# Kernel tuning notes

Measured on AMD Instinct MI355X. Metric: run time of the kernel, lower is better.

Reference implementation:

```python
import jax, jax.numpy as jnp
from jax import lax
import numpy as np

D_MODEL = 2048
NUM_EXPERTS = 16
NUM_TOKENS = 8192  # must be divisible by NUM_EXPERTS (balanced assignment)


def setup_inputs() -> dict:
    key = jax.random.key(0)
    k1, k2 = jax.random.split(key)
    features = jax.random.normal(k1, (NUM_TOKENS, D_MODEL), dtype=jnp.float32)
    # gate weight (orthogonal init in torch; gaussian is fine for a numerical baseline)
    W = jax.random.normal(k2, (NUM_EXPERTS, D_MODEL), dtype=jnp.float32) * 0.1
    b = jnp.zeros((NUM_EXPERTS,), dtype=jnp.float32)
    return {"features": features, "W": W, "b": b, "is_training": 1}


def _balanced_assignment(scores):
    """Greedy balanced assignment: each expert receives exactly T//E tokens.
    Deterministic stand-in for the cpp auction-based balanced_assignment: scan
    over tokens, each token takes its best-scoring expert with remaining capacity.
    Returns sort_by_expert: token indices sorted (stably) by assigned expert."""
    T, E = scores.shape
    cap_per_expert = T // E

    def step(cap, s):  # cap: [E] remaining capacity, s: [E] token's scores
        masked = jnp.where(cap > 0, s, -jnp.inf)
        e = jnp.argmax(masked)
        return cap.at[e].add(-1), e

    _, tok2exp = lax.scan(step, jnp.full((E,), cap_per_expert, dtype=jnp.int32), scores)
    sort_by_expert = jnp.argsort(tok2exp, stable=True)  # [T] token ids grouped by expert
    return sort_by_expert


def reference(features, W, b, is_training):
    # gating computed under no_grad in the original
    affinities = lax.stop_gradient(features @ W.T + b)  # [T, E]
    T, E = affinities.shape
    cap = T // E

    sort_by_expert = _balanced_assignment(affinities)

    routing_probs = jax.nn.softmax(affinities, axis=1)  # [T, E]

    # gather_scores: permute probs into expert order, pick each token's score for
    # its assigned expert, then un-permute back to original token order.
    sorted_probs = routing_probs[sort_by_expert]                 # [T, E]
    expert_idx = (jnp.arange(T) // cap)[:, None]                 # [T, 1], balanced splits
    gathered = jnp.take_along_axis(sorted_probs, expert_idx, axis=1)  # [T, 1]
    i_sort = jnp.argsort(sort_by_expert)                         # inverse permutation
    gathered_scores = gathered[i_sort]                           # [T, 1]

    return sort_by_expert, gathered_scores
```

## Files before the change

### kernel.cpp

```cpp
#include <hip/hip_runtime.h>
#include <hip/hip_bf16.h>
#include <math.h>

#define T_TOK 8192
#define D_MODEL 2048
#define N_EXP 16
#define CAP 512
#define NSEG (T_TOK / 64)


__device__ __forceinline__ unsigned int f2ord(float f) {
    unsigned int b = __float_as_uint(f);
    return (b & 0x80000000u) ? ~b : (b | 0x80000000u);
}

__global__ __launch_bounds__(512, 4) void gemm_aff_kernel(
    const float* __restrict__ feat, const float* __restrict__ W,
    float* __restrict__ aff)
{
    __shared__ float flds[8][D_MODEL];

    const int tid  = threadIdx.x;
    const int wave = tid >> 6, lane = tid & 63;
    const int tbase = blockIdx.x * 8;

    {
        const float4* src = (const float4*)(feat + (size_t)tbase * D_MODEL);
        float4* dst = (float4*)&flds[0][0];
        #pragma unroll
        for (int i = 0; i < 8; ++i)
            dst[tid + i * 512] = src[tid + i * 512];
    }

    const float* w0 = W + (size_t)(wave * 2) * D_MODEL + lane * 4;
    const float* w1 = w0 + D_MODEL;

    float acc[16];
    #pragma unroll
    for (int i = 0; i < 16; ++i) acc[i] = 0.f;

    float4 wv0 = *(const float4*)(w0);
    float4 wv1 = *(const float4*)(w1);
    __syncthreads();

    #pragma unroll
    for (int j = 0; j < 8; ++j) {
        float4 wn0, wn1;
        if (j < 7) {
            wn0 = *(const float4*)(w0 + (j + 1) * 256);
            wn1 = *(const float4*)(w1 + (j + 1) * 256);
        } else {
            wn0 = wv0; wn1 = wv1;
        }
        const float* fl = &flds[0][0] + j * 256 + lane * 4;
        #pragma unroll
        for (int r = 0; r < 8; ++r) {
            float4 f = *(const float4*)(fl + r * D_MODEL);
            acc[r * 2 + 0] += f.x * wv0.x;
            acc[r * 2 + 0] += f.y * wv0.y;
            acc[r * 2 + 0] += f.z * wv0.z;
            acc[r * 2 + 0] += f.w * wv0.w;
            acc[r * 2 + 1] += f.x * wv1.x;
            acc[r * 2 + 1] += f.y * wv1.y;
            acc[r * 2 + 1] += f.z * wv1.z;
            acc[r * 2 + 1] += f.w * wv1.w;
        }
        wv0 = wn0; wv1 = wn1;
    }

    #pragma unroll
    for (int step = 0; step < 4; ++step) {
        const int m    = 1 << step;
        const int half = 8 >> step;
        const bool hi  = (lane & m) != 0;
        #pragma unroll
        for (int jj = 0; jj < half; ++jj) {
            float send = hi ? acc[jj] : acc[jj + half];
            float recv = __shfl_xor(send, m, 64);
            acc[jj] = (hi ? acc[jj + half] : acc[jj]) + recv;
        }
    }
    acc[0] += __shfl_xor(acc[0], 16, 64);
    acc[0] += __shfl_xor(acc[0], 32, 64);

    if (lane < 16) {
        const int slot = ((lane & 1) << 3) | (((lane >> 1) & 1) << 2)
                       | (((lane >> 2) & 1) << 1) | ((lane >> 3) & 1);
        const int r = slot >> 1, el = slot & 1;
        aff[(size_t)(tbase + r) * N_EXP + wave * 2 + el] = acc[0];
    }
}

__global__ __launch_bounds__(256) void finalize_kernel(
    const float* __restrict__ aff_in, const float* __restrict__ bias,
    unsigned long long* __restrict__ pref, float* __restrict__ probs)
{
    const int t = blockIdx.x * 256 + threadIdx.x;

    float aff[N_EXP];
    const float4* p = (const float4*)(aff_in + (size_t)t * N_EXP);
    #pragma unroll
    for (int q = 0; q < 4; ++q) {
        float4 v = p[q];
        aff[q*4+0] = v.x; aff[q*4+1] = v.y; aff[q*4+2] = v.z; aff[q*4+3] = v.w;
    }
    #pragma unroll
    for (int e = 0; e < N_EXP; ++e) aff[e] += bias[e];

    float m = aff[0];
    #pragma unroll
    for (int e = 1; e < N_EXP; ++e) m = fmaxf(m, aff[e]);
    float s = 0.f;
    #pragma unroll
    for (int e = 0; e < N_EXP; ++e) s += __expf(aff[e] - m);

    float4* pr = (float4*)(probs + (size_t)t * N_EXP);
    #pragma unroll
    for (int q = 0; q < 4; ++q) {
        float4 v;
        v.x = __expf(aff[q*4+0] - m) / s;
        v.y = __expf(aff[q*4+1] - m) / s;
        v.z = __expf(aff[q*4+2] - m) / s;
        v.w = __expf(aff[q*4+3] - m) / s;
        pr[q] = v;
    }

    unsigned long long key[N_EXP];
    #pragma unroll
    for (int j = 0; j < N_EXP; ++j)
        key[j] = ((unsigned long long)f2ord(aff[j]) << 4) | (unsigned long long)(15 - j);
    unsigned long long pk = 0ull;
    unsigned int used = 0;
    for (int r = 0; r < N_EXP; ++r) {
        unsigned long long bk = 0ull; int be = 0;
        for (int j = 0; j < N_EXP; ++j)
            if (!((used >> j) & 1u) && key[j] > bk) { bk = key[j]; be = j; }
        used |= (1u << be);
        pk = (pk << 4) | (unsigned long long)be;
    }
    pref[t] = pk;
}

__global__ __launch_bounds__(512, 1) void events_kernel(
    const unsigned long long* __restrict__ pref, int* __restrict__ evt)
{
    __shared__ unsigned long long segmask[N_EXP][NSEG];
    __shared__ int fparr[N_EXP];

    const int tid  = threadIdx.x;
    const int wave = tid >> 6, lane = tid & 63;
    const unsigned long long lt_mask = (1ull << lane) - 1ull;

    unsigned long long myPref[16];
    #pragma unroll
    for (int k = 0; k < 16; ++k) myPref[k] = pref[tid + 512 * k];

    #pragma unroll
    for (int k = 0; k < 16; ++k) {
        const int s = k * 8 + wave;
        const int c = (int)(myPref[k] >> 60);
        #pragma unroll
        for (int e = 0; e < N_EXP; ++e) {
            unsigned long long mm = __ballot(c == e);
            if (lane == e) segmask[e][s] = mm;
        }
    }
    __syncthreads();

    const int eA = wave, eB = wave + 8;
    int capA = CAP, capB = CAP;
    unsigned long long m0A = 0, m1A = 0, m0B = 0, m1B = 0;
    int excl0A = 0, excl1A = 0, excl0B = 0, excl1B = 0;
    int segF = 0;
    unsigned long long mlep = 0;
    unsigned int avail = 0xFFFFu;
    int myp = 0, myf = 0;

    for (int round = 0; round < N_EXP; ++round) {
        {
            int exf = (segF < 64) ? __shfl(excl0A, segF, 64) : __shfl(excl1A, segF - 64, 64);
            unsigned long long mf = (segF < 64) ? __shfl(m0A, segF, 64) : __shfl(m1A, segF - 64, 64);
            capA -= exf + (int)__popcll(mf & mlep);
            exf = (segF < 64) ? __shfl(excl0B, segF, 64) : __shfl(excl1B, segF - 64, 64);
            mf  = (segF < 64) ? __shfl(m0B, segF, 64) : __shfl(m1B, segF - 64, 64);
            capB -= exf + (int)__popcll(mf & mlep);
        }

        unsigned long long a0 = segmask[eA][lane];
        unsigned long long a1 = segmask[eA][64 + lane];
        unsigned long long b0 = segmask[eB][lane];
        unsigned long long b1 = segmask[eB][64 + lane];
        if (lane < segF)            { a0 = 0; b0 = 0; }
        else if (lane == segF)      { a0 &= ~mlep; b0 &= ~mlep; }
        if (64 + lane < segF)       { a1 = 0; b1 = 0; }
        else if (64 + lane == segF) { a1 &= ~mlep; b1 &= ~mlep; }
        m0A = a0; m1A = a1; m0B = b0; m1B = b1;

        const int c0A = (int)__popcll(a0), c1A = (int)__popcll(a1);
        const int c0B = (int)__popcll(b0), c1B = (int)__popcll(b1);
        int v0A = c0A, v1A = c1A, v0B = c0B, v1B = c1B;
        #pragma unroll
        for (int d = 1; d < 64; d <<= 1) {
            int t0 = __shfl_up(v0A, d, 64);
            int t1 = __shfl_up(v1A, d, 64);
            int t2 = __shfl_up(v0B, d, 64);
            int t3 = __shfl_up(v1B, d, 64);
            if (lane >= d) { v0A += t0; v1A += t1; v0B += t2; v1B += t3; }
        }
        const int tot0A = __shfl(v0A, 63, 64);
        const int tot0B = __shfl(v0B, 63, 64);
        excl0A = v0A - c0A;
        excl1A = tot0A + v1A - c1A;
        excl0B = v0B - c0B;
        excl1B = tot0B + v1B - c1B;

        int fpA = 0x7FFFFFFF;
        if ((avail >> eA) & 1u) {
            const int need = capA;
            int segc = -1, kk = 0;
            if (excl0A < need && excl0A + c0A >= need)      { segc = lane;      kk = need - excl0A; }
            else if (excl1A < need && excl1A + c1A >= need) { segc = 64 + lane; kk = need - excl1A; }
            unsigned long long bb = __ballot(segc >= 0);
            if (bb) {
                int l2    = __builtin_ctzll(bb);
                int sstar = __shfl(segc, l2, 64);
                int k2    = __shfl(kk,   l2, 64);
                unsigned long long msel = (sstar < 64) ? __shfl(a0, sstar, 64)
                                                       : __shfl(a1, sstar - 64, 64);
                int rr = (int)__popcll(msel & lt_mask);
                bool hit = ((msel >> lane) & 1ull) && (rr == k2 - 1);
                unsigned long long hb = __ballot(hit);
                fpA = sstar * 64 + __builtin_ctzll(hb);
            }
        }
        int fpB = 0x7FFFFFFF;
        if ((avail >> eB) & 1u) {
            const int need = capB;
            int segc = -1, kk = 0;
            if (excl0B < need && excl0B + c0B >= need)      { segc = lane;      kk = need - excl0B; }
            else if (excl1B < need && excl1B + c1B >= need) { segc = 64 + lane; kk = need - excl1B; }
            unsigned long long bb = __ballot(segc >= 0);
            if (bb) {
                int l2    = __builtin_ctzll(bb);
                int sstar = __shfl(segc, l2, 64);
                int k2    = __shfl(kk,   l2, 64);
                unsigned long long msel = (sstar < 64) ? __shfl(b0, sstar, 64)
                                                       : __shfl(b1, sstar - 64, 64);
                int rr = (int)__popcll(msel & lt_mask);
                bool hit = ((msel >> lane) & 1ull) && (rr == k2 - 1);
                unsigned long long hb = __ballot(hit);
                fpB = sstar * 64 + __builtin_ctzll(hb);
            }
        }
        if (lane == 0) { fparr[eA] = fpA; fparr[eB] = fpB; }
        __syncthreads();

        int pmin = 0x7FFFFFFF, fe = 0;
        #pragma unroll
        for (int e = 0; e < N_EXP; ++e) {
            int f = fparr[e];
            if (f < pmin) { pmin = f; fe = e; }
        }
        if (tid == round) { myp = pmin; myf = fe; }

        const int nsegF = pmin >> 6;
        const unsigned long long nmlep = ((pmin & 63) == 63) ? ~0ull
                                         : ((1ull << ((pmin & 63) + 1)) - 1ull);
        const unsigned int navail = avail & ~(1u << fe);

        if (round < N_EXP - 1) {
            #pragma unroll
            for (int k = 0; k < 16; ++k) {
                const int s = k * 8 + wave;
                if (s >= nsegF) {
                    unsigned long long m = segmask[fe][s];
                    if (s == nsegF) m &= ~nmlep;
                    if ((m >> lane) & 1ull) {
                        unsigned long long pp = myPref[k];
                        int e2 = (int)(pp >> 60);
                        while (!((navail >> e2) & 1u)) { pp <<= 4; e2 = (int)(pp >> 60); }
                        atomicOr(&segmask[e2][s], 1ull << lane);
                    }
                }
            }
        }
        segF = nsegF; mlep = nmlep; avail = navail;
        __syncthreads();
    }

    if (tid < N_EXP) { evt[tid] = myp; evt[N_EXP + tid] = myf; }
}

__global__ __launch_bounds__(256) void choice_kernel(
    const unsigned long long* __restrict__ pref, const int* __restrict__ evt,
    unsigned char* __restrict__ t2e, int* __restrict__ bcnt)
{
    __shared__ int evp[N_EXP], evf[N_EXP];
    __shared__ int sc[4][N_EXP];
    const int tid = threadIdx.x, b = blockIdx.x;
    const int wave = tid >> 6, lane = tid & 63;
    if (tid < N_EXP) evp[tid] = evt[tid];
    else if (tid < 2 * N_EXP) evf[tid - N_EXP] = evt[tid];
    __syncthreads();

    const int t = b * 256 + tid;
    unsigned int mask = 0xFFFFu;
    #pragma unroll
    for (int j = 0; j < N_EXP; ++j)
        if (evp[j] < t) mask &= ~(1u << evf[j]);

    unsigned long long pp = pref[t];
    int e = (int)(pp >> 60);
    while (!((mask >> e) & 1u)) { pp <<= 4; e = (int)(pp >> 60); }
    t2e[t] = (unsigned char)e;

    #pragma unroll
    for (int e2 = 0; e2 < N_EXP; ++e2) {
        unsigned long long mm = __ballot(e == e2);
        if (lane == e2) sc[wave][e2] = (int)__popcll(mm);
    }
    __syncthreads();
    if (tid < N_EXP)
        bcnt[b * N_EXP + tid] = sc[0][tid] + sc[1][tid] + sc[2][tid] + sc[3][tid];
}

__global__ __launch_bounds__(256) void writeout_kernel(
    const unsigned char* __restrict__ t2e, const int* __restrict__ bcnt,
    const float* __restrict__ probs,
    float* __restrict__ out0, float* __restrict__ out1)
{
    __shared__ int base[N_EXP];
    __shared__ int sc[4][N_EXP];
    const int tid = threadIdx.x, b = blockIdx.x;
    const int wave = tid >> 6, lane = tid & 63;
    const unsigned long long lt_mask = (1ull << lane) - 1ull;

    const int t = b * 256 + tid;
    const int c = (int)t2e[t];

    unsigned long long own = 0ull;
    #pragma unroll
    for (int e2 = 0; e2 < N_EXP; ++e2) {
        unsigned long long mm = __ballot(c == e2);
        if (c == e2) own = mm;
        if (lane == e2) sc[wave][e2] = (int)__popcll(mm);
    }
    if (tid < N_EXP) {
        int s = 0;
        for (int b2 = 0; b2 < b; ++b2) s += bcnt[b2 * N_EXP + tid];
        base[tid] = s;
    }
    __syncthreads();

    int rank = (int)__popcll(own & lt_mask);
    for (int w2 = 0; w2 < wave; ++w2) rank += sc[w2][c];
    const int pos = base[c] + rank;
    out0[c * CAP + pos] = (float)t;
    out1[t] = probs[(size_t)t * N_EXP + c];
}

extern "C" void kernel_launch(void* const* d_in, const int* in_sizes, int n_in,
                              void* d_out, int out_size, void* d_ws, size_t ws_size,
                              hipStream_t stream) {
    const float* feat = (const float*)d_in[0];
    const float* W    = (const float*)d_in[1];
    const float* bias = (const float*)d_in[2];

    float* out = (float*)d_out;
    char*  ws  = (char*)d_ws;

    float* aff               = (float*)ws;
    unsigned long long* pref = (unsigned long long*)(ws + 524288);
    float* probs             = (float*)(ws + 589824);
    int* evt                 = (int*)(ws + 1114112);
    unsigned char* t2e       = (unsigned char*)(ws + 1114240);
    int* bcnt                = (int*)(ws + 1122432);

    hipLaunchKernelGGL(gemm_aff_kernel, dim3(T_TOK / 8), dim3(512), 0, stream,
                       feat, W, aff);
    hipLaunchKernelGGL(finalize_kernel, dim3(T_TOK / 256), dim3(256), 0, stream,
                       aff, bias, pref, probs);
    hipLaunchKernelGGL(events_kernel, dim3(1), dim3(512), 0, stream,
                       pref, evt);
    hipLaunchKernelGGL(choice_kernel, dim3(T_TOK / 256), dim3(256), 0, stream,
                       pref, evt, t2e, bcnt);
    hipLaunchKernelGGL(writeout_kernel, dim3(T_TOK / 256), dim3(256), 0, stream,
                       t2e, bcnt, probs, out, out + T_TOK);
}
```

Baseline: 185.6 us.

## Fuse softmax/preference into GEMM and merge choice with writeout via grid sync

```diff
diff --git a/kernel.cpp b/kernel.cpp
--- a/kernel.cpp
+++ b/kernel.cpp
@@ -14,11 +14,13 @@
     return (b & 0x80000000u) ? ~b : (b | 0x80000000u);
 }
 
-__global__ __launch_bounds__(512, 4) void gemm_aff_kernel(
+__global__ __launch_bounds__(512, 4) void gemm_finalize_kernel(
     const float* __restrict__ feat, const float* __restrict__ W,
-    float* __restrict__ aff)
+    const float* __restrict__ bias,
+    unsigned long long* __restrict__ pref, float* __restrict__ probs)
 {
     __shared__ float flds[8][D_MODEL];
+    __shared__ float afft[8][N_EXP];
 
     const int tid  = threadIdx.x;
     const int wave = tid >> 6, lane = tid & 63;
@@ -87,62 +89,48 @@
         const int slot = ((lane & 1) << 3) | (((lane >> 1) & 1) << 2)
                        | (((lane >> 2) & 1) << 1) | ((lane >> 3) & 1);
         const int r = slot >> 1, el = slot & 1;
-        aff[(size_t)(tbase + r) * N_EXP + wave * 2 + el] = acc[0];
-    }
-}
-
-__global__ __launch_bounds__(256) void finalize_kernel(
-    const float* __restrict__ aff_in, const float* __restrict__ bias,
-    unsigned long long* __restrict__ pref, float* __restrict__ probs)
-{
-    const int t = blockIdx.x * 256 + threadIdx.x;
-
-    float aff[N_EXP];
-    const float4* p = (const float4*)(aff_in + (size_t)t * N_EXP);
-    #pragma unroll
-    for (int q = 0; q < 4; ++q) {
-        float4 v = p[q];
-        aff[q*4+0] = v.x; aff[q*4+1] = v.y; aff[q*4+2] = v.z; aff[q*4+3] = v.w;
-    }
-    #pragma unroll
-    for (int e = 0; e < N_EXP; ++e) aff[e] += bias[e];
-
-    float m = aff[0];
-    #pragma unroll
-    for (int e = 1; e < N_EXP; ++e) m = fmaxf(m, aff[e]);
+        afft[r][wave * 2 + el] = acc[0];
+    }
+    __syncthreads();
+
+    const int tk = tbase + wave;
+    const int j  = lane & 15;
+    float v = afft[wave][j] + bias[j];
+
+    float mx = v;
+    #pragma unroll
+    for (int d = 1; d < 16; d <<= 1)
+        mx = fmaxf(mx, __shfl_xor(mx, d, 16));
+
+    float ex = __expf(v - mx);
+
     float s = 0.f;
     #pragma unroll
-    for (int e = 0; e < N_EXP; ++e) s += __expf(aff[e] - m);
-
-    float4* pr = (float4*)(probs + (size_t)t * N_EXP);
-    #pragma unroll
-    for (int q = 0; q < 4; ++q) {
-        float4 v;
-        v.x = __expf(aff[q*4+0] - m) / s;
-        v.y = __expf(aff[q*4+1] - m) / s;
-        v.z = __expf(aff[q*4+2] - m) / s;
-        v.w = __expf(aff[q*4+3] - m) / s;
-        pr[q] = v;
-    }
-
-    unsigned long long key[N_EXP];
-    #pragma unroll
-    for (int j = 0; j < N_EXP; ++j)
-        key[j] = ((unsigned long long)f2ord(aff[j]) << 4) | (unsigned long long)(15 - j);
-    unsigned long long pk = 0ull;
-    unsigned int used = 0;
-    for (int r = 0; r < N_EXP; ++r) {
-        unsigned long long bk = 0ull; int be = 0;
-        for (int j = 0; j < N_EXP; ++j)
-            if (!((used >> j) & 1u) && key[j] > bk) { bk = key[j]; be = j; }
-        used |= (1u << be);
-        pk = (pk << 4) | (unsigned long long)be;
-    }
-    pref[t] = pk;
+    for (int e2 = 0; e2 < N_EXP; ++e2)
+        s += __shfl(ex, e2, 16);
+
+    if (lane < 16)
+        probs[(size_t)tk * N_EXP + lane] = ex / s;
+
+    unsigned long long key = ((unsigned long long)f2ord(v) << 4)
+                           | (unsigned long long)(15 - j);
+    int rank = 0;
+    #pragma unroll
+    for (int d = 1; d < 16; ++d) {
+        unsigned long long o = __shfl_xor(key, d, 16);
+        rank += (o > key) ? 1 : 0;
+    }
+    unsigned long long contrib = ((unsigned long long)j) << (4 * (15 - rank));
+    #pragma unroll
+    for (int d = 1; d < 16; d <<= 1)
+        contrib |= __shfl_xor(contrib, d, 16);
+    if (lane == 0)
+        pref[tk] = contrib;
 }
 
 __global__ __launch_bounds__(512, 1) void events_kernel(
-    const unsigned long long* __restrict__ pref, int* __restrict__ evt)
+    const unsigned long long* __restrict__ pref, int* __restrict__ evt,
+    int* __restrict__ gsync)
 {
     __shared__ unsigned long long segmask[N_EXP][NSEG];
     __shared__ int fparr[N_EXP];
@@ -150,6 +138,8 @@
     const int tid  = threadIdx.x;
     const int wave = tid >> 6, lane = tid & 63;
     const unsigned long long lt_mask = (1ull << lane) - 1ull;
+
+    if (tid == 0) *gsync = 0;
 
     unsigned long long myPref[16];
     #pragma unroll
@@ -291,14 +281,18 @@
     if (tid < N_EXP) { evt[tid] = myp; evt[N_EXP + tid] = myf; }
 }
 
-__global__ __launch_bounds__(256) void choice_kernel(
+__global__ __launch_bounds__(256) void choice_write_kernel(
     const unsigned long long* __restrict__ pref, const int* __restrict__ evt,
-    unsigned char* __restrict__ t2e, int* __restrict__ bcnt)
+    const float* __restrict__ probs, int* __restrict__ bcnt, int* __restrict__ gsync,
+    float* __restrict__ out0, float* __restrict__ out1)
 {
     __shared__ int evp[N_EXP], evf[N_EXP];
     __shared__ int sc[4][N_EXP];
+    __shared__ int base[N_EXP];
     const int tid = threadIdx.x, b = blockIdx.x;
     const int wave = tid >> 6, lane = tid & 63;
+    const unsigned long long lt_mask = (1ull << lane) - 1ull;
+
     if (tid < N_EXP) evp[tid] = evt[tid];
     else if (tid < 2 * N_EXP) evf[tid - N_EXP] = evt[tid];
     __syncthreads();
@@ -306,57 +300,46 @@
     const int t = b * 256 + tid;
     unsigned int mask = 0xFFFFu;
     #pragma unroll
-    for (int j = 0; j < N_EXP; ++j)
-        if (evp[j] < t) mask &= ~(1u << evf[j]);
+    for (int jj = 0; jj < N_EXP; ++jj)
+        if (evp[jj] < t) mask &= ~(1u << evf[jj]);
 
     unsigned long long pp = pref[t];
     int e = (int)(pp >> 60);
     while (!((mask >> e) & 1u)) { pp <<= 4; e = (int)(pp >> 60); }
-    t2e[t] = (unsigned char)e;
-
+
+    unsigned long long own = 0ull;
     #pragma unroll
     for (int e2 = 0; e2 < N_EXP; ++e2) {
         unsigned long long mm = __ballot(e == e2);
+        if (e == e2) own = mm;
         if (lane == e2) sc[wave][e2] = (int)__popcll(mm);
     }
     __syncthreads();
+
     if (tid < N_EXP)
-        bcnt[b * N_EXP + tid] = sc[0][tid] + sc[1][tid] + sc[2][tid] + sc[3][tid];
-}
-
-__global__ __launch_bounds__(256) void writeout_kernel(
-    const unsigned char* __restrict__ t2e, const int* __restrict__ bcnt,
-    const float* __restrict__ probs,
-    float* __restrict__ out0, float* __restrict__ out1)
-{
-    __shared__ int base[N_EXP];
-    __shared__ int sc[4][N_EXP];
-    const int tid = threadIdx.x, b = blockIdx.x;
-    const int wave = tid >> 6, lane = tid & 63;
-    const unsigned long long lt_mask = (1ull << lane) - 1ull;
-
-    const int t = b * 256 + tid;
-    const int c = (int)t2e[t];
-
-    unsigned long long own = 0ull;
-    #pragma unroll
-    for (int e2 = 0; e2 < N_EXP; ++e2) {
-        unsigned long long mm = __ballot(c == e2);
-        if (c == e2) own = mm;
-        if (lane == e2) sc[wave][e2] = (int)__popcll(mm);
-    }
+        atomicExch(&bcnt[b * N_EXP + tid],
+                   sc[0][tid] + sc[1][tid] + sc[2][tid] + sc[3][tid]);
+    __syncthreads();
+
+    if (tid == 0) {
+        __threadfence();
+        atomicAdd(gsync, 1);
+        while (atomicAdd(gsync, 0) < 32) { __builtin_amdgcn_s_sleep(2); }
+    }
+    __syncthreads();
+
     if (tid < N_EXP) {
         int s = 0;
-        for (int b2 = 0; b2 < b; ++b2) s += bcnt[b2 * N_EXP + tid];
+        for (int b2 = 0; b2 < b; ++b2) s += atomicAdd(&bcnt[b2 * N_EXP + tid], 0);
         base[tid] = s;
     }
     __syncthreads();
 
     int rank = (int)__popcll(own & lt_mask);
-    for (int w2 = 0; w2 < wave; ++w2) rank += sc[w2][c];
-    const int pos = base[c] + rank;
-    out0[c * CAP + pos] = (float)t;
-    out1[t] = probs[(size_t)t * N_EXP + c];
+    for (int w2 = 0; w2 < wave; ++w2) rank += sc[w2][e];
+    const int pos = base[e] + rank;
+    out0[e * CAP + pos] = (float)t;
+    out1[t] = probs[(size_t)t * N_EXP + e];
 }
 
 extern "C" void kernel_launch(void* const* d_in, const int* in_sizes, int n_in,
@@ -369,21 +352,16 @@
     float* out = (float*)d_out;
     char*  ws  = (char*)d_ws;
 
-    float* aff               = (float*)ws;
     unsigned long long* pref = (unsigned long long*)(ws + 524288);
     float* probs             = (float*)(ws + 589824);
     int* evt                 = (int*)(ws + 1114112);
-    unsigned char* t2e       = (unsigned char*)(ws + 1114240);
+    int* gsync               = (int*)(ws + 1114240);
     int* bcnt                = (int*)(ws + 1122432);
 
-    hipLaunchKernelGGL(gemm_aff_kernel, dim3(T_TOK / 8), dim3(512), 0, stream,
-                       feat, W, aff);
-    hipLaunchKernelGGL(finalize_kernel, dim3(T_TOK / 256), dim3(256), 0, stream,
-                       aff, bias, pref, probs);
+    hipLaunchKernelGGL(gemm_finalize_kernel, dim3(T_TOK / 8), dim3(512), 0, stream,
+                       feat, W, bias, pref, probs);
     hipLaunchKernelGGL(events_kernel, dim3(1), dim3(512), 0, stream,
-                       pref, evt);
-    hipLaunchKernelGGL(choice_kernel, dim3(T_TOK / 256), dim3(256), 0, stream,
-                       pref, evt, t2e, bcnt);
-    hipLaunchKernelGGL(writeout_kernel, dim3(T_TOK / 256), dim3(256), 0, stream,
-                       t2e, bcnt, probs, out, out + T_TOK);
-}
+                       pref, evt, gsync);
+    hipLaunchKernelGGL(choice_write_kernel, dim3(T_TOK / 256), dim3(256), 0, stream,
+                       pref, evt, probs, bcnt, gsync, out, out + T_TOK);
+}
```

New measurement: 182.5 us. About the same (-1.7%).
